# Kernel tuning notes

Measured on AMD Instinct MI355X. Metric: run time of the kernel, lower is better.

Reference implementation:

```python
import jax, jax.numpy as jnp
import numpy as np

B, S, H = 2, 2048, 2048
NH, NKV, HD = 32, 8, 64          # num_heads, num_kv_heads, head_dim
G = NH // NKV                     # GQA group size
NEG = -1e9


def setup_inputs() -> dict:
    key = jax.random.key(0)
    ks = jax.random.split(key, 8)
    x = jax.random.normal(ks[0], (B, S, H), dtype=jnp.float32)
    # real RoPE frequencies: theta = 10000 ** (-2i/hd)
    inv_freq = 1.0 / (10000.0 ** (np.arange(0, HD, 2, dtype=np.float32) / HD))
    angles = np.arange(S, dtype=np.float32)[:, None] * inv_freq[None, :]  # [S, HD//2]
    freqs_cos = jnp.asarray(np.cos(angles))
    freqs_sin = jnp.asarray(np.sin(angles))
    # additive causal mask [S, S]
    mask = jnp.where(jnp.tril(jnp.ones((S, S), dtype=bool)), 0.0, NEG).astype(jnp.float32)
    sc = 0.02
    Wq = jax.random.normal(ks[1], (NH * HD, H), dtype=jnp.float32) * sc
    bq = jax.random.normal(ks[2], (NH * HD,), dtype=jnp.float32) * sc
    Wk = jax.random.normal(ks[3], (NKV * HD, H), dtype=jnp.float32) * sc
    bk = jax.random.normal(ks[4], (NKV * HD,), dtype=jnp.float32) * sc
    Wv = jax.random.normal(ks[5], (NKV * HD, H), dtype=jnp.float32) * sc
    bv = jax.random.normal(ks[6], (NKV * HD,), dtype=jnp.float32) * sc
    Wo = jax.random.normal(ks[7], (H, NH * HD), dtype=jnp.float32) * sc
    return {"x": x, "freqs_cos": freqs_cos, "freqs_sin": freqs_sin, "mask": mask,
            "Wq": Wq, "bq": bq, "Wk": Wk, "bk": bk, "Wv": Wv, "bv": bv, "Wo": Wo}


def _rotate_half(t):
    h = t.shape[-1] // 2
    return jnp.concatenate([-t[..., h:], t[..., :h]], axis=-1)


def reference(x, freqs_cos, freqs_sin, mask, Wq, bq, Wk, bk, Wv, bv, Wo):
    b, s, _ = x.shape
    q = (x @ Wq.T + bq).reshape(b, s, NH, HD)
    k = (x @ Wk.T + bk).reshape(b, s, NKV, HD)
    v = (x @ Wv.T + bv).reshape(b, s, NKV, HD)
    # RoPE (rotate_half style): cos/sin duplicated along last dim -> [1, s, 1, HD]
    cos = jnp.concatenate([freqs_cos, freqs_cos], axis=-1)[None, :, None, :]
    sin = jnp.concatenate([freqs_sin, freqs_sin], axis=-1)[None, :, None, :]
    q = q * cos + _rotate_half(q) * sin
    k = k * cos + _rotate_half(k) * sin
    # GQA: view q as [b, s, NKV, G, HD]; avoids repeat_interleave of K/V (same math)
    q5 = q.reshape(b, s, NKV, G, HD)
    scores = jnp.einsum('bqhgd,bkhd->bhgqk', q5, k) / jnp.sqrt(jnp.float32(HD))
    scores = scores + mask  # broadcast [s, s] over [b, h, g, s, s]
    p = jax.nn.softmax(scores.astype(jnp.float32), axis=-1).astype(q.dtype)
    out = jnp.einsum('bhgqk,bkhd->bqhgd', p, v).reshape(b, s, NH * HD)
    return out @ Wo.T
```

## Files before the change

kernel.cpp:

```cpp
#include <hip/hip_runtime.h>
#include <hip/hip_bf16.h>
#include <cstddef>
#include <cstdint>

#define B_   2
#define S_   2048
#define H_   2048
#define NH_  32
#define NKV_ 8
#define HD_  64

typedef __attribute__((ext_vector_type(8))) short short8;
typedef __attribute__((ext_vector_type(4))) float v4f;
typedef __attribute__((ext_vector_type(16))) float v16f;

#define MAXC 48.0f
#define QSCALE 0.18033688011112042f

__device__ __forceinline__ unsigned short f2b(float f) {
    unsigned int u = __float_as_uint(f);
    u += 0x7FFFu + ((u >> 16) & 1u);
    return (unsigned short)(u >> 16);
}
__device__ __forceinline__ unsigned int pkbf(float a, float b) {
    __hip_bfloat162 h = __float22bfloat162_rn(float2{a, b});
    return *(unsigned int*)&h;
}
__device__ __forceinline__ v4f mfma16(short8 a, short8 b, v4f c) {
    return __builtin_amdgcn_mfma_f32_16x16x32_bf16(a, b, c, 0, 0, 0);
}
__device__ __forceinline__ v16f mfma32(short8 a, short8 b, v16f c) {
    return __builtin_amdgcn_mfma_f32_32x32x16_bf16(a, b, c, 0, 0, 0);
}
__device__ __forceinline__ void gll16(void* lds, const void* g) {
    __builtin_amdgcn_global_load_lds(
        (const __attribute__((address_space(1))) unsigned int*)g,
        (__attribute__((address_space(3))) unsigned int*)lds, 16, 0, 0);
}

__global__ __launch_bounds__(256) void convert_all(
    const float* __restrict__ x, const float* __restrict__ wq,
    const float* __restrict__ wk, const float* __restrict__ wv,
    const float* __restrict__ wo,
    unsigned short* __restrict__ xb, unsigned short* __restrict__ wqb,
    unsigned short* __restrict__ wkb, unsigned short* __restrict__ wvb,
    unsigned short* __restrict__ wob)
{
    size_t i = ((size_t)blockIdx.x * 256 + threadIdx.x) * 4;
    const float* src; unsigned short* dst; size_t off;
    if (i < 8388608)       { src = x;  dst = xb;  off = i; }
    else if (i < 12582912) { src = wq; dst = wqb; off = i - 8388608; }
    else if (i < 13631488) { src = wk; dst = wkb; off = i - 12582912; }
    else if (i < 14680064) { src = wv; dst = wvb; off = i - 13631488; }
    else                   { src = wo; dst = wob; off = i - 14680064; }
    float4 v = *(const float4*)(src + off);
    ushort4 o;
    o.x = f2b(v.x); o.y = f2b(v.y); o.z = f2b(v.z); o.w = f2b(v.w);
    *(ushort4*)(dst + off) = o;
}

__global__ __launch_bounds__(256) void qkv_gemm(
    const unsigned short* __restrict__ xb,
    const unsigned short* __restrict__ wqb, const unsigned short* __restrict__ wkb,
    const unsigned short* __restrict__ wvb,
    const float* __restrict__ bq, const float* __restrict__ bk,
    const float* __restrict__ bv,
    const float* __restrict__ fc, const float* __restrict__ fs,
    unsigned short* __restrict__ Qb, unsigned short* __restrict__ Kb,
    unsigned short* __restrict__ Vt)
{
    __shared__ unsigned short As[128 * 64];
    __shared__ unsigned short Bs[128 * 64];
    const int tid = threadIdx.x;
    const int lane = tid & 63, w = tid >> 6;
    const int tx = lane & 15, quad = lane >> 4;
    const int bx = blockIdx.x, by = blockIdx.y;

    const unsigned short *Ap, *Bp;
    int mode, aBase, bBase;
    if (bx < 16)      { mode = 0; Ap = xb;  Bp = wqb; aBase = by * 128; bBase = bx * 128; }
    else if (bx < 20) { mode = 1; Ap = xb;  Bp = wkb; aBase = by * 128; bBase = (bx - 16) * 128; }
    else              { mode = 2; Ap = wvb; Bp = xb;  aBase = (bx - 20) * 128; bBase = by * 128; }

    const int wm = (w >> 1) * 64, wn = (w & 1) * 64;
    v4f acc[4][4];
#pragma unroll
    for (int i = 0; i < 4; ++i)
#pragma unroll
        for (int j = 0; j < 4; ++j) acc[i][j] = (v4f)0.f;

    const int r8 = lane >> 3, gc = (lane & 7) ^ r8;
    const unsigned short* ga = &Ap[(size_t)(aBase + w * 32 + r8) * 2048 + gc * 8];
    const unsigned short* gb = &Bp[(size_t)(bBase + w * 32 + r8) * 2048 + gc * 8];

    const int t7 = tx & 7;
    int slA[2], slB[2];
#pragma unroll
    for (int kk = 0; kk < 2; ++kk) { slA[kk] = ((kk * 4 + quad) ^ t7) * 8; slB[kk] = slA[kk]; }

    for (int k0 = 0; k0 < 2048; k0 += 64) {
        __syncthreads();
#pragma unroll
        for (int i = 0; i < 4; ++i) {
            gll16(&As[(w * 32 + i * 8) * 64], ga + (size_t)(i * 8) * 2048 + k0);
            gll16(&Bs[(w * 32 + i * 8) * 64], gb + (size_t)(i * 8) * 2048 + k0);
        }
        __syncthreads();
#pragma unroll
        for (int kk = 0; kk < 2; ++kk) {
            short8 af[4], bf[4];
#pragma unroll
            for (int mt = 0; mt < 4; ++mt)
                af[mt] = *(const short8*)&As[(wm + mt * 16 + tx) * 64 + slA[kk]];
#pragma unroll
            for (int nt = 0; nt < 4; ++nt)
                bf[nt] = *(const short8*)&Bs[(wn + nt * 16 + tx) * 64 + slB[kk]];
#pragma unroll
            for (int mt = 0; mt < 4; ++mt)
#pragma unroll
                for (int nt = 0; nt < 4; ++nt)
                    acc[mt][nt] = mfma16(af[mt], bf[nt], acc[mt][nt]);
        }
    }

    if (mode <= 1) {
        unsigned short* Cout = mode ? Kb : Qb;
        const float* bias    = mode ? bk : bq;
        const int ldN        = mode ? 512 : 2048;
        const float scq      = mode ? 1.0f : QSCALE;
        float bx0 = bias[bBase + wn +  0 + tx];
        float bx1 = bias[bBase + wn + 16 + tx];
        float bx2 = bias[bBase + wn + 32 + tx];
        float bx3 = bias[bBase + wn + 48 + tx];
#pragma unroll
        for (int mt = 0; mt < 4; ++mt)
#pragma unroll
            for (int rg = 0; rg < 4; ++rg) {
                int m = aBase + wm + mt * 16 + quad * 4 + rg;
                int s = m & (S_ - 1);
                float c0 = fc[s * 32 + tx],      c1 = fc[s * 32 + 16 + tx];
                float s0 = fs[s * 32 + tx],      s1 = fs[s * 32 + 16 + tx];
                float q0 = acc[mt][0][rg] + bx0, q1 = acc[mt][1][rg] + bx1;
                float q2 = acc[mt][2][rg] + bx2, q3 = acc[mt][3][rg] + bx3;
                size_t base = (size_t)m * ldN + bBase + wn + tx;
                Cout[base]      = f2b((q0 * c0 - q2 * s0) * scq);
                Cout[base + 16] = f2b((q1 * c1 - q3 * s1) * scq);
                Cout[base + 32] = f2b((q2 * c0 + q0 * s0) * scq);
                Cout[base + 48] = f2b((q3 * c1 + q1 * s1) * scq);
            }
    } else {
#pragma unroll
        for (int mt = 0; mt < 4; ++mt)
#pragma unroll
            for (int rg = 0; rg < 4; ++rg) {
                int d = aBase + wm + mt * 16 + quad * 4 + rg;
                float bvv = bv[d];
                size_t base = (size_t)d * 4096 + bBase + wn + tx;
#pragma unroll
                for (int nt = 0; nt < 4; ++nt)
                    Vt[base + nt * 16] = f2b(acc[mt][nt][rg] + bvv);
            }
    }
}

__global__ __launch_bounds__(256) void out_gemm(
    const unsigned short* __restrict__ Ab, const unsigned short* __restrict__ Bw,
    float* __restrict__ C)
{
    __shared__ unsigned short As[128 * 64];
    __shared__ unsigned short Bs[128 * 64];
    const int tid = threadIdx.x;
    const int lane = tid & 63, w = tid >> 6;
    const int tx = lane & 15, quad = lane >> 4;
    const int bm = blockIdx.y * 128, bn = blockIdx.x * 128;
    const int wm = (w >> 1) * 64, wn = (w & 1) * 64;

    v4f acc[4][4];
#pragma unroll
    for (int i = 0; i < 4; ++i)
#pragma unroll
        for (int j = 0; j < 4; ++j) acc[i][j] = (v4f)0.f;

    const int r8 = lane >> 3, gc = (lane & 7) ^ r8;
    const unsigned short* ga = &Ab[(size_t)(bm + w * 32 + r8) * 2048 + gc * 8];
    const unsigned short* gb = &Bw[(size_t)(bn + w * 32 + r8) * 2048 + gc * 8];
    const int t7 = tx & 7;
    int sl[2];
#pragma unroll
    for (int kk = 0; kk < 2; ++kk) sl[kk] = ((kk * 4 + quad) ^ t7) * 8;

    for (int k0 = 0; k0 < 2048; k0 += 64) {
        __syncthreads();
#pragma unroll
        for (int i = 0; i < 4; ++i) {
            gll16(&As[(w * 32 + i * 8) * 64], ga + (size_t)(i * 8) * 2048 + k0);
            gll16(&Bs[(w * 32 + i * 8) * 64], gb + (size_t)(i * 8) * 2048 + k0);
        }
        __syncthreads();
#pragma unroll
        for (int kk = 0; kk < 2; ++kk) {
            short8 af[4], bf[4];
#pragma unroll
            for (int mt = 0; mt < 4; ++mt)
                af[mt] = *(const short8*)&As[(wm + mt * 16 + tx) * 64 + sl[kk]];
#pragma unroll
            for (int nt = 0; nt < 4; ++nt)
                bf[nt] = *(const short8*)&Bs[(wn + nt * 16 + tx) * 64 + sl[kk]];
#pragma unroll
            for (int mt = 0; mt < 4; ++mt)
#pragma unroll
                for (int nt = 0; nt < 4; ++nt)
                    acc[mt][nt] = mfma16(af[mt], bf[nt], acc[mt][nt]);
        }
    }
#pragma unroll
    for (int mt = 0; mt < 4; ++mt)
#pragma unroll
        for (int nt = 0; nt < 4; ++nt)
#pragma unroll
            for (int rg = 0; rg < 4; ++rg) {
                int m = bm + wm + mt * 16 + quad * 4 + rg;
                C[(size_t)m * 2048 + bn + wn + nt * 16 + tx] = acc[mt][nt][rg];
            }
}

__global__ __launch_bounds__(128) void attn_mfma(
    const unsigned short* __restrict__ Q, const unsigned short* __restrict__ K,
    const unsigned short* __restrict__ Vt, unsigned short* __restrict__ O)
{
    __shared__ __align__(16) unsigned short Ks[64 * 72];
    __shared__ __align__(16) unsigned short Vs[64 * 72];
    const int tid = threadIdx.x;
    const int lane = tid & 63, wq = tid >> 6;
    const int l32 = lane & 31, half = lane >> 5;
    const int h = blockIdx.y, b = blockIdx.z;
    const int T = (blockIdx.x + 4 * (h >> 3) + 16 * b) & 31;
    const int kvh = h >> 2;
    const int qh = wq;

    const int qrow = T * 64 + qh * 32 + l32;
    const unsigned short* Qr = &Q[(((size_t)b * S_ + qrow) * NH_ + h) * HD_];
    short8 qf[4];
#pragma unroll
    for (int s = 0; s < 4; ++s)
        qf[s] = *(const short8*)(Qr + s * 16 + half * 8);

    float l = 0.f;
    v16f o0 = (v16f)0.f, o1 = (v16f)0.f;

    for (int kt = 0; kt <= T; ++kt) {
        __syncthreads();
#pragma unroll
        for (int i = 0; i < 4; ++i) {
            int e = tid + i * 128;
            int row = e >> 3, c8 = (e & 7) * 8;
            *(uint4*)&Ks[row * 72 + c8] =
                *(const uint4*)&K[(((size_t)b * S_ + kt * 64 + row) * NKV_ + kvh) * HD_ + c8];
            *(uint4*)&Vs[row * 72 + c8] =
                *(const uint4*)&Vt[(size_t)(kvh * 64 + row) * 4096 + b * 2048 + kt * 64 + c8];
        }
        __syncthreads();
        const bool diag = (kt == T);
        const int tpart = diag ? qh : 2;

        for (int t = 0; t < 2; ++t) {
            if (diag && t > tpart) break;
            const int kb = (t * 32 + l32) * 72 + half * 8;
            v16f st = (v16f)(-MAXC);
            __builtin_amdgcn_s_setprio(1);
            st = mfma32(*(const short8*)&Ks[kb],      qf[0], st);
            st = mfma32(*(const short8*)&Ks[kb + 16], qf[1], st);
            st = mfma32(*(const short8*)&Ks[kb + 32], qf[2], st);
            st = mfma32(*(const short8*)&Ks[kb + 48], qf[3], st);
            __builtin_amdgcn_s_setprio(0);
            const bool part = diag && (t == tpart);
            float pv[16];
#pragma unroll
            for (int r = 0; r < 16; ++r) {
                int krow = (r & 3) + 8 * (r >> 2) + 4 * half;
                bool msk = part && (krow > l32);
                pv[r] = msk ? 0.f : exp2f(st[r]);
                l += pv[r];
            }
            unsigned int u[8];
#pragma unroll
            for (int g = 0; g < 4; ++g) {
                u[2 * g]     = pkbf(pv[4 * g],     pv[4 * g + 1]);
                u[2 * g + 1] = pkbf(pv[4 * g + 2], pv[4 * g + 3]);
            }
#pragma unroll
            for (int sg = 0; sg < 2; ++sg) {
                unsigned int a0 = u[4 * sg], a1 = u[4 * sg + 1];
                unsigned int b0 = u[4 * sg + 2], b1 = u[4 * sg + 3];
                unsigned int s0 = __shfl_xor((int)a0, 32);
                unsigned int s1 = __shfl_xor((int)a1, 32);
                unsigned int s2 = __shfl_xor((int)b0, 32);
                unsigned int s3 = __shfl_xor((int)b1, 32);
                uint4 fw;
                fw.x = half ? s2 : a0;
                fw.y = half ? s3 : a1;
                fw.z = half ? b0 : s0;
                fw.w = half ? b1 : s1;
                short8 pf = *(short8*)&fw;
                const int vo = (2 * t + sg) * 16 + half * 8;
                __builtin_amdgcn_s_setprio(1);
                o0 = mfma32(*(const short8*)&Vs[l32 * 72 + vo],        pf, o0);
                o1 = mfma32(*(const short8*)&Vs[(32 + l32) * 72 + vo], pf, o1);
                __builtin_amdgcn_s_setprio(0);
            }
        }
    }

    l += __shfl_xor(l, 32);
    float inv = 1.f / l;
    int qg = T * 64 + qh * 32 + l32;
    unsigned short* orow = &O[((size_t)b * S_ + qg) * (NH_ * HD_) + h * HD_];
#pragma unroll
    for (int td = 0; td < 2; ++td) {
        const v16f& oo = td ? o1 : o0;
#pragma unroll
        for (int g = 0; g < 4; ++g) {
            int d = td * 32 + g * 8 + half * 4;
            uint2 uu;
            uu.x = pkbf(oo[4 * g] * inv,     oo[4 * g + 1] * inv);
            uu.y = pkbf(oo[4 * g + 2] * inv, oo[4 * g + 3] * inv);
            *(uint2*)&orow[d] = uu;
        }
    }
}

extern "C" void kernel_launch(void* const* d_in, const int* in_sizes, int n_in,
                              void* d_out, int out_size, void* d_ws, size_t ws_size,
                              hipStream_t stream)
{
    const float* x  = (const float*)d_in[0];
    const float* fc = (const float*)d_in[1];
    const float* fs = (const float*)d_in[2];
    const float* Wq = (const float*)d_in[4];
    const float* bq = (const float*)d_in[5];
    const float* Wk = (const float*)d_in[6];
    const float* bk = (const float*)d_in[7];
    const float* Wv = (const float*)d_in[8];
    const float* bv = (const float*)d_in[9];
    const float* Wo = (const float*)d_in[10];
    float* out = (float*)d_out;

    unsigned short* ws = (unsigned short*)d_ws;
    unsigned short* xb  = ws;
    unsigned short* wqb = ws + 8388608;
    unsigned short* wkb = ws + 12582912;
    unsigned short* wvb = ws + 13631488;
    unsigned short* wob = ws + 14680064;
    unsigned short* Qb  = ws + 18874368;
    unsigned short* Kb  = ws + 27262976;
    unsigned short* Vt  = ws + 29360128;
    unsigned short* Ob  = ws + 31457280;

    dim3 blk(256);
    convert_all<<<18432, blk, 0, stream>>>(x, Wq, Wk, Wv, Wo, xb, wqb, wkb, wvb, wob);
    qkv_gemm<<<dim3(24, 32), blk, 0, stream>>>(xb, wqb, wkb, wvb, bq, bk, bv,
                                               fc, fs, Qb, Kb, Vt);
    attn_mfma<<<dim3(32, NH_, B_), dim3(128), 0, stream>>>(Qb, Kb, Vt, Ob);
    out_gemm<<<dim3(16, 32), blk, 0, stream>>>(Ob, wob, out);
}
```

Before: 355.9 us.

## Split KV tile across wave pairs and pair causal query tiles per block

The attention kernel now uses 256 threads. Waves are split along the key dimension of each 64-key tile, and each block processes two query tiles (p and 31-p) so causal work is balanced across blocks. Partial outputs and row sums from the two key-halves are reduced through shared memory before writing. It also uses permlane32_swap instead of four shuffles when available and splits the row-sum accumulation into independent partial sums. The cost is an extra shared-memory reduction and added syncs per query tile.

Result: faster. 334.4 us (-6.0%).

```diff
diff --git a/kernel.cpp b/kernel.cpp
--- a/kernel.cpp
+++ b/kernel.cpp
@@ -224,48 +224,53 @@
             }
 }
 
-__global__ __launch_bounds__(128) void attn_mfma(
+__global__ __launch_bounds__(256) void attn_mfma(
     const unsigned short* __restrict__ Q, const unsigned short* __restrict__ K,
     const unsigned short* __restrict__ Vt, unsigned short* __restrict__ O)
 {
-    __shared__ __align__(16) unsigned short Ks[64 * 72];
-    __shared__ __align__(16) unsigned short Vs[64 * 72];
+    __shared__ __align__(16) unsigned short smem[2 * 64 * 72];
+    unsigned short* Ks = smem;
+    unsigned short* Vs = smem + 64 * 72;
     const int tid = threadIdx.x;
     const int lane = tid & 63, wq = tid >> 6;
     const int l32 = lane & 31, half = lane >> 5;
+    const int qh = wq & 1;
+    const int ts = wq >> 1;
+    const int p = blockIdx.x;
     const int h = blockIdx.y, b = blockIdx.z;
-    const int T = (blockIdx.x + 4 * (h >> 3) + 16 * b) & 31;
     const int kvh = h >> 2;
-    const int qh = wq;
-
-    const int qrow = T * 64 + qh * 32 + l32;
-    const unsigned short* Qr = &Q[(((size_t)b * S_ + qrow) * NH_ + h) * HD_];
-    short8 qf[4];
-#pragma unroll
-    for (int s = 0; s < 4; ++s)
-        qf[s] = *(const short8*)(Qr + s * 16 + half * 8);
-
-    float l = 0.f;
-    v16f o0 = (v16f)0.f, o1 = (v16f)0.f;
-
-    for (int kt = 0; kt <= T; ++kt) {
-        __syncthreads();
-#pragma unroll
-        for (int i = 0; i < 4; ++i) {
-            int e = tid + i * 128;
-            int row = e >> 3, c8 = (e & 7) * 8;
-            *(uint4*)&Ks[row * 72 + c8] =
-                *(const uint4*)&K[(((size_t)b * S_ + kt * 64 + row) * NKV_ + kvh) * HD_ + c8];
-            *(uint4*)&Vs[row * 72 + c8] =
-                *(const uint4*)&Vt[(size_t)(kvh * 64 + row) * 4096 + b * 2048 + kt * 64 + c8];
-        }
-        __syncthreads();
-        const bool diag = (kt == T);
-        const int tpart = diag ? qh : 2;
-
-        for (int t = 0; t < 2; ++t) {
-            if (diag && t > tpart) break;
-            const int kb = (t * 32 + l32) * 72 + half * 8;
+
+    const int srow = tid >> 3, sc8 = (tid & 7) * 8;
+
+    for (int ph = 0; ph < 2; ++ph) {
+        const int T = ph ? (31 - p) : p;
+
+        const int qrow = T * 64 + qh * 32 + l32;
+        const unsigned short* Qr = &Q[(((size_t)b * S_ + qrow) * NH_ + h) * HD_];
+        short8 qf[4];
+#pragma unroll
+        for (int s = 0; s < 4; ++s)
+            qf[s] = *(const short8*)(Qr + s * 16 + half * 8);
+
+        float la = 0.f, lb = 0.f, lc = 0.f, ld = 0.f;
+        v16f o0 = (v16f)0.f, o1 = (v16f)0.f;
+
+        for (int kt = 0; kt <= T; ++kt) {
+            __syncthreads();
+#pragma unroll
+            for (int i = 0; i < 2; ++i) {
+                int row = srow + i * 32;
+                *(uint4*)&Ks[row * 72 + sc8] =
+                    *(const uint4*)&K[(((size_t)b * S_ + kt * 64 + row) * NKV_ + kvh) * HD_ + sc8];
+                *(uint4*)&Vs[row * 72 + sc8] =
+                    *(const uint4*)&Vt[(size_t)(kvh * 64 + row) * 4096 + b * 2048 + kt * 64 + sc8];
+            }
+            __syncthreads();
+            const bool diag = (kt == T);
+            if (diag && ts > qh) continue;
+            const bool part = diag && (ts == qh);
+
+            const int kb = (ts * 32 + l32) * 72 + half * 8;
             v16f st = (v16f)(-MAXC);
             __builtin_amdgcn_s_setprio(1);
             st = mfma32(*(const short8*)&Ks[kb],      qf[0], st);
@@ -273,15 +278,22 @@
             st = mfma32(*(const short8*)&Ks[kb + 32], qf[2], st);
             st = mfma32(*(const short8*)&Ks[kb + 48], qf[3], st);
             __builtin_amdgcn_s_setprio(0);
-            const bool part = diag && (t == tpart);
+
             float pv[16];
 #pragma unroll
-            for (int r = 0; r < 16; ++r) {
-                int krow = (r & 3) + 8 * (r >> 2) + 4 * half;
-                bool msk = part && (krow > l32);
-                pv[r] = msk ? 0.f : exp2f(st[r]);
-                l += pv[r];
-            }
+            for (int r = 0; r < 16; ++r) pv[r] = exp2f(st[r]);
+            if (part) {
+#pragma unroll
+                for (int r = 0; r < 16; ++r) {
+                    int krow = (r & 3) + 8 * (r >> 2) + 4 * half;
+                    if (krow > l32) pv[r] = 0.f;
+                }
+            }
+            la += (pv[0]  + pv[1])  + (pv[2]  + pv[3]);
+            lb += (pv[4]  + pv[5])  + (pv[6]  + pv[7]);
+            lc += (pv[8]  + pv[9])  + (pv[10] + pv[11]);
+            ld += (pv[12] + pv[13]) + (pv[14] + pv[15]);
+
             unsigned int u[8];
 #pragma unroll
             for (int g = 0; g < 4; ++g) {
@@ -292,39 +304,62 @@
             for (int sg = 0; sg < 2; ++sg) {
                 unsigned int a0 = u[4 * sg], a1 = u[4 * sg + 1];
                 unsigned int b0 = u[4 * sg + 2], b1 = u[4 * sg + 3];
+                uint4 fw;
+#if __has_builtin(__builtin_amdgcn_permlane32_swap)
+                typedef unsigned int u2v __attribute__((ext_vector_type(2)));
+                u2v r0 = __builtin_amdgcn_permlane32_swap(a0, b0, false, false);
+                u2v r1 = __builtin_amdgcn_permlane32_swap(a1, b1, false, false);
+                fw.x = r0[0]; fw.y = r1[0]; fw.z = r0[1]; fw.w = r1[1];
+#else
                 unsigned int s0 = __shfl_xor((int)a0, 32);
                 unsigned int s1 = __shfl_xor((int)a1, 32);
                 unsigned int s2 = __shfl_xor((int)b0, 32);
                 unsigned int s3 = __shfl_xor((int)b1, 32);
-                uint4 fw;
                 fw.x = half ? s2 : a0;
                 fw.y = half ? s3 : a1;
                 fw.z = half ? b0 : s0;
                 fw.w = half ? b1 : s1;
+#endif
                 short8 pf = *(short8*)&fw;
-                const int vo = (2 * t + sg) * 16 + half * 8;
+                const int vo = (2 * ts + sg) * 16 + half * 8;
                 __builtin_amdgcn_s_setprio(1);
                 o0 = mfma32(*(const short8*)&Vs[l32 * 72 + vo],        pf, o0);
                 o1 = mfma32(*(const short8*)&Vs[(32 + l32) * 72 + vo], pf, o1);
                 __builtin_amdgcn_s_setprio(0);
             }
         }
-    }
-
-    l += __shfl_xor(l, 32);
-    float inv = 1.f / l;
-    int qg = T * 64 + qh * 32 + l32;
-    unsigned short* orow = &O[((size_t)b * S_ + qg) * (NH_ * HD_) + h * HD_];
-#pragma unroll
-    for (int td = 0; td < 2; ++td) {
-        const v16f& oo = td ? o1 : o0;
-#pragma unroll
-        for (int g = 0; g < 4; ++g) {
-            int d = td * 32 + g * 8 + half * 4;
-            uint2 uu;
-            uu.x = pkbf(oo[4 * g] * inv,     oo[4 * g + 1] * inv);
-            uu.y = pkbf(oo[4 * g + 2] * inv, oo[4 * g + 3] * inv);
-            *(uint2*)&orow[d] = uu;
+
+        float l = (la + lb) + (lc + ld);
+        l += __shfl_xor(l, 32);
+
+        __syncthreads();
+        float* red = (float*)smem;
+        const int rbase = (qh * 64 + lane) * 33;
+        if (ts == 1) {
+#pragma unroll
+            for (int r = 0; r < 16; ++r) { red[rbase + r] = o0[r]; red[rbase + 16 + r] = o1[r]; }
+            red[rbase + 32] = l;
+        }
+        __syncthreads();
+        if (ts == 0) {
+#pragma unroll
+            for (int r = 0; r < 16; ++r) { o0[r] += red[rbase + r]; o1[r] += red[rbase + 16 + r]; }
+            l += red[rbase + 32];
+            float inv = 1.f / l;
+            int qg = T * 64 + qh * 32 + l32;
+            unsigned short* orow = &O[((size_t)b * S_ + qg) * (NH_ * HD_) + h * HD_];
+#pragma unroll
+            for (int td = 0; td < 2; ++td) {
+                const v16f& oo = td ? o1 : o0;
+#pragma unroll
+                for (int g = 0; g < 4; ++g) {
+                    int d = td * 32 + g * 8 + half * 4;
+                    uint2 uu;
+                    uu.x = pkbf(oo[4 * g] * inv,     oo[4 * g + 1] * inv);
+                    uu.y = pkbf(oo[4 * g + 2] * inv, oo[4 * g + 3] * inv);
+                    *(uint2*)&orow[d] = uu;
+                }
+            }
         }
     }
 }
@@ -360,6 +395,6 @@
     convert_all<<<18432, blk, 0, stream>>>(x, Wq, Wk, Wv, Wo, xb, wqb, wkb, wvb, wob);
     qkv_gemm<<<dim3(24, 32), blk, 0, stream>>>(xb, wqb, wkb, wvb, bq, bk, bv,
                                                fc, fs, Qb, Kb, Vt);
-    attn_mfma<<<dim3(32, NH_, B_), dim3(128), 0, stream>>>(Qb, Kb, Vt, Ob);
+    attn_mfma<<<dim3(16, NH_, B_), blk, 0, stream>>>(Qb, Kb, Vt, Ob);
     out_gemm<<<dim3(16, 32), blk, 0, stream>>>(Ob, wob, out);
 }
```
